# Kernel optimization log

Hardware: AMD Instinct MI355X
Metric: run time of the kernel (lower is better)

## Reference

```python
import jax, jax.numpy as jnp
import numpy as np

C = 128
K = 23
D = 3
ALPHA = 0.5
K_D = max(1, K // D)          # 7
S = 2 * D - 1                 # 5
C4 = C // 4 if C >= 4 else 1  # 32


def dwconv(x, w, pad, dil):
    # x: [B,C,H,W], w: [C,1,kh,kw] depthwise (groups=C)
    return jax.lax.conv_general_dilated(
        x, w, window_strides=(1, 1), padding=pad, rhs_dilation=dil,
        dimension_numbers=('NCHW', 'OIHW', 'NCHW'),
        feature_group_count=x.shape[1])


def setup_inputs() -> dict:
    key = jax.random.key(0)
    ks = jax.random.split(key, 10)
    sc = 0.1
    return {
        'x': jax.random.normal(ks[0], (4, C, 256, 256), jnp.float32),
        'h1_w': jax.random.normal(ks[1], (C, 1, 1, S), jnp.float32) * sc,
        'h2_w': jax.random.normal(ks[2], (C, 1, 1, K_D), jnp.float32) * sc,
        'v1_w': jax.random.normal(ks[3], (C, 1, S, 1), jnp.float32) * sc,
        'v2_w': jax.random.normal(ks[4], (C, 1, K_D, 1), jnp.float32) * sc,
        'g1_w': jax.random.normal(ks[5], (C4, 2 * C), jnp.float32) * sc,
        'g2_w': jax.random.normal(ks[6], (2, C4), jnp.float32) * sc,
        'g2_b': jnp.zeros((2,), jnp.float32),
        'fuse_w': jax.random.normal(ks[7], (C, C), jnp.float32) * sc,
        'fuse_b': jnp.zeros((C,), jnp.float32),
    }


def reference(x, h1_w, h2_w, v1_w, v2_w, g1_w, g2_w, g2_b, fuse_w, fuse_b):
    # directional depthwise large-kernel paths
    h = dwconv(x, h1_w, [(0, 0), (S // 2, S // 2)], (1, 1))
    h = dwconv(h, h2_w, [(0, 0), ((K_D - 1) * D // 2, (K_D - 1) * D // 2)], (1, D))
    v = dwconv(x, v1_w, [(S // 2, S // 2), (0, 0)], (1, 1))
    v = dwconv(v, v2_w, [((K_D - 1) * D // 2, (K_D - 1) * D // 2), (0, 0)], (D, 1))
    # gate: global avg pool over concat[h, v] -> 1x1 MLP -> softmax over 2 dirs
    pooled = jnp.concatenate([h.mean(axis=(2, 3)), v.mean(axis=(2, 3))], axis=1)  # [B, 2C]
    g = pooled @ g1_w.T
    g = g * jax.nn.sigmoid(g)  # SiLU
    w = jax.nn.softmax(g @ g2_w.T + g2_b, axis=1)  # [B, 2]
    wh = w[:, 0][:, None, None, None]
    wv = w[:, 1][:, None, None, None]
    attn = wh * h + wv * v
    # 1x1 fuse conv
    attn = jnp.einsum('bchw,oc->bohw', attn, fuse_w) + fuse_b[None, :, None, None]
    y = x * attn
    return x + ALPHA * (y - x)
```

## Files before the change

kernel.cpp:

```cpp
#include <hip/hip_runtime.h>
#include <hip/hip_bf16.h>

#define CCH 128
#define HGT 256
#define WID 256
#define HW  65536

typedef __attribute__((ext_vector_type(8))) short short8;
typedef __attribute__((ext_vector_type(4))) float floatx4;


__global__ __launch_bounds__(256) void prep_kernel(float* __restrict__ sums) {
  int t = threadIdx.x;
  for (int i = t; i < 1032; i += 256) sums[i] = 0.f;
}

__global__ __launch_bounds__(256) void convh_kernel(
    const float* __restrict__ x, const float* __restrict__ h1w,
    const float* __restrict__ h2w,
    __hip_bfloat16* __restrict__ hbuf, float* __restrict__ sum_h) {
  __shared__ float xr[16 * 260];
  __shared__ float tmp[16 * 276];
  __shared__ float red[4];
  int bid = blockIdx.x;
  int y0 = (bid & 15) * 16;
  int bc = bid >> 4;
  int c = bc & (CCH - 1);
  int t = threadIdx.x;
  int rowg = t >> 6;
  int c4 = (t & 63) * 4;

  if (t < 64) {
    int r = t >> 2, k = t & 3;
    int col = (k < 2) ? k : (256 + k);
    xr[r * 260 + col] = 0.f;
  }
  for (int i = t; i < 288; i += 256) {
    int r = i / 18, k = i - r * 18;
    int col = (k < 9) ? k : (256 + k);
    tmp[r * 276 + col] = 0.f;
  }

  const float* xg = x + (size_t)bc * HW + (size_t)y0 * WID;
#pragma unroll
  for (int k = 0; k < 4; ++k) {
    int r = 4 * k + rowg;
    float4 v = *(const float4*)(xg + (size_t)r * WID + c4);
    *(float2*)&xr[r * 260 + 2 + c4] = make_float2(v.x, v.y);
    *(float2*)&xr[r * 260 + 4 + c4] = make_float2(v.z, v.w);
  }
  float h1c[5], h2c[7];
#pragma unroll
  for (int i = 0; i < 5; ++i) h1c[i] = h1w[c * 5 + i];
#pragma unroll
  for (int j = 0; j < 7; ++j) h2c[j] = h2w[c * 7 + j];
  __syncthreads();

#pragma unroll
  for (int r = 0; r < 16; ++r) {
    float s1 = 0.f;
#pragma unroll
    for (int i = 0; i < 5; ++i) s1 = fmaf(xr[r * 260 + t + i], h1c[i], s1);
    tmp[r * 276 + 9 + t] = s1;
  }
  __syncthreads();

  __hip_bfloat16* hg = hbuf + (size_t)bc * HW + (size_t)y0 * WID + t;
  float acc = 0.f;
#pragma unroll
  for (int r = 0; r < 16; ++r) {
    float s = 0.f;
#pragma unroll
    for (int j = 0; j < 7; ++j) s = fmaf(tmp[r * 276 + t + 3 * j], h2c[j], s);
    hg[(size_t)r * WID] = __float2bfloat16(s);
    acc += s;
  }
#pragma unroll
  for (int off = 32; off > 0; off >>= 1) acc += __shfl_down(acc, off);
  if ((t & 63) == 0) red[t >> 6] = acc;
  __syncthreads();
  if (t == 0) atomicAdd(&sum_h[bc], red[0] + red[1] + red[2] + red[3]);
}

__global__ __launch_bounds__(256) void convv_kernel(
    const float* __restrict__ x, const float* __restrict__ v1w,
    const float* __restrict__ v2w,
    __hip_bfloat16* __restrict__ vbuf, float* __restrict__ sum_v) {
  int bid = blockIdx.x;
  int half = bid & 1;
  int bc = bid >> 1;
  int c = bc & (CCH - 1);
  int t = threadIdx.x;
  int y0 = half * 128;
  const float* xp = x + (size_t)bc * HW;
  float v1c[5], v2c[7];
#pragma unroll
  for (int i = 0; i < 5; ++i) v1c[i] = v1w[c * 5 + i];
#pragma unroll
  for (int j = 0; j < 7; ++j) v2c[j] = v2w[c * 7 + j];

  float xloc[23];
#pragma unroll
  for (int m = 0; m < 23; ++m) {
    int yy = y0 - 11 + m;
    xloc[m] = (yy >= 0 && yy < HGT) ? xp[(size_t)yy * WID + t] : 0.f;
  }
  float s1w[19];
#pragma unroll
  for (int m = 0; m < 19; ++m) {
    int q = y0 - 9 + m;
    float v = 0.f;
    if (q >= 0 && q < HGT) {
#pragma unroll
      for (int i = 0; i < 5; ++i) v = fmaf(xloc[m + i], v1c[i], v);
    }
    s1w[m] = v;
  }
  float xw[5];
#pragma unroll
  for (int i = 0; i < 5; ++i) {
    int yy = y0 + 8 + i;
    xw[i] = (yy >= 0 && yy < HGT) ? xp[(size_t)yy * WID + t] : 0.f;
  }

  __hip_bfloat16* vp = vbuf + (size_t)bc * HW;
  float acc = 0.f;
  for (int y = y0; y < y0 + 128; ++y) {
    float s = 0.f;
#pragma unroll
    for (int j = 0; j < 7; ++j) s = fmaf(s1w[3 * j], v2c[j], s);
    vp[(size_t)y * WID + t] = __float2bfloat16(s);
    acc += s;
#pragma unroll
    for (int m = 0; m < 18; ++m) s1w[m] = s1w[m + 1];
    int q = y + 10;
    float ns = 0.f;
    if (q < HGT) {
#pragma unroll
      for (int i = 0; i < 5; ++i) ns = fmaf(xw[i], v1c[i], ns);
    }
    s1w[18] = ns;
#pragma unroll
    for (int i = 0; i < 4; ++i) xw[i] = xw[i + 1];
    int yy = y + 13;
    xw[4] = (yy < HGT) ? xp[(size_t)yy * WID + t] : 0.f;
  }
  __shared__ float red[4];
#pragma unroll
  for (int off = 32; off > 0; off >>= 1) acc += __shfl_down(acc, off);
  if ((t & 63) == 0) red[t >> 6] = acc;
  __syncthreads();
  if (t == 0) atomicAdd(&sum_v[bc], red[0] + red[1] + red[2] + red[3]);
}

__global__ __launch_bounds__(128) void gate_kernel(
    const float* __restrict__ sum_h, const float* __restrict__ sum_v,
    const float* __restrict__ g1w, const float* __restrict__ g2w,
    const float* __restrict__ g2b, float* __restrict__ wgate) {
  int t = threadIdx.x;
  __shared__ float gs[4][32];
  int b = t >> 5, r = t & 31;
  {
    float acc = 0.f;
    const float inv = 1.f / 65536.f;
    for (int k = 0; k < 128; ++k)
      acc = fmaf(sum_h[b * 128 + k] * inv, g1w[r * 256 + k], acc);
    for (int k = 0; k < 128; ++k)
      acc = fmaf(sum_v[b * 128 + k] * inv, g1w[r * 256 + 128 + k], acc);
    float sig = 1.f / (1.f + expf(-acc));
    gs[b][r] = acc * sig;
  }
  __syncthreads();
  if (t < 4) {
    float t0 = g2b[0], t1 = g2b[1];
    for (int rr = 0; rr < 32; ++rr) {
      t0 = fmaf(gs[t][rr], g2w[rr], t0);
      t1 = fmaf(gs[t][rr], g2w[32 + rr], t1);
    }
    float mx = fmaxf(t0, t1);
    float e0 = expf(t0 - mx), e1 = expf(t1 - mx);
    float inv = 1.f / (e0 + e1);
    wgate[t * 2 + 0] = e0 * inv;
    wgate[t * 2 + 1] = e1 * inv;
  }
}

__device__ __forceinline__ float bf2f(unsigned short u) {
  return __uint_as_float(((unsigned)u) << 16);
}
__device__ __forceinline__ short f2bfs(float f) {
  return (short)__bfloat16_as_ushort(__float2bfloat16(f));
}

__global__ __launch_bounds__(256, 4) void fuse_kernel(
    const float* __restrict__ x, const __hip_bfloat16* __restrict__ hbuf,
    const __hip_bfloat16* __restrict__ vbuf, const float* __restrict__ fuse_w,
    const float* __restrict__ fuse_b, const float* __restrict__ wgate,
    float* __restrict__ out) {
  __shared__ unsigned short aT[128 * 128];
  int bid = blockIdx.x;
  int half = bid & 1;
  int y = (bid >> 1) & 255;
  int b = bid >> 9;
  int t = threadIdx.x;
  int w = t >> 6, lane = t & 63;
  int quad = lane >> 4, n16 = lane & 15;
  float wh = wgate[b * 2], wv = wgate[b * 2 + 1];

  short8 wf[2][4];
#pragma unroll
  for (int mi = 0; mi < 2; ++mi) {
    int o = (2 * w + mi) * 16 + n16;
#pragma unroll
    for (int kt = 0; kt < 4; ++kt) {
      const float* wp = fuse_w + o * 128 + kt * 32 + quad * 8;
      float4 f0 = *(const float4*)wp;
      float4 f1 = *(const float4*)(wp + 4);
      short8 s;
      s[0] = f2bfs(f0.x); s[1] = f2bfs(f0.y); s[2] = f2bfs(f0.z); s[3] = f2bfs(f0.w);
      s[4] = f2bfs(f1.x); s[5] = f2bfs(f1.y); s[6] = f2bfs(f1.z); s[7] = f2bfs(f1.w);
      wf[mi][kt] = s;
    }
  }

  size_t base = (size_t)(b * CCH) * HW + (size_t)y * WID + half * 128;
  const unsigned short* hb = (const unsigned short*)hbuf;
  const unsigned short* vb = (const unsigned short*)vbuf;
  int cth = t >> 4;
  int p0 = (t & 15) * 8;
  int swz = 8 * (t & 15);
#pragma unroll
  for (int cpass = 0; cpass < 8; ++cpass) {
    int c = cpass * 16 + cth;
    size_t gi = base + (size_t)c * HW + p0;
    ushort4 h0 = *(const ushort4*)(hb + gi);
    ushort4 h1 = *(const ushort4*)(hb + gi + 4);
    ushort4 v0 = *(const ushort4*)(vb + gi);
    ushort4 v1 = *(const ushort4*)(vb + gi + 4);
    int cpr = (c + swz) & 127;
    float a0 = fmaf(wh, bf2f(h0.x), wv * bf2f(v0.x));
    float a1 = fmaf(wh, bf2f(h0.y), wv * bf2f(v0.y));
    float a2 = fmaf(wh, bf2f(h0.z), wv * bf2f(v0.z));
    float a3 = fmaf(wh, bf2f(h0.w), wv * bf2f(v0.w));
    float a4 = fmaf(wh, bf2f(h1.x), wv * bf2f(v1.x));
    float a5 = fmaf(wh, bf2f(h1.y), wv * bf2f(v1.y));
    float a6 = fmaf(wh, bf2f(h1.z), wv * bf2f(v1.z));
    float a7 = fmaf(wh, bf2f(h1.w), wv * bf2f(v1.w));
    aT[(p0 + 0) * 128 + cpr] = (unsigned short)f2bfs(a0);
    aT[(p0 + 1) * 128 + cpr] = (unsigned short)f2bfs(a1);
    aT[(p0 + 2) * 128 + cpr] = (unsigned short)f2bfs(a2);
    aT[(p0 + 3) * 128 + cpr] = (unsigned short)f2bfs(a3);
    aT[(p0 + 4) * 128 + cpr] = (unsigned short)f2bfs(a4);
    aT[(p0 + 5) * 128 + cpr] = (unsigned short)f2bfs(a5);
    aT[(p0 + 6) * 128 + cpr] = (unsigned short)f2bfs(a6);
    aT[(p0 + 7) * 128 + cpr] = (unsigned short)f2bfs(a7);
  }
  __syncthreads();

  floatx4 acc[2][8];
#pragma unroll
  for (int mi = 0; mi < 2; ++mi)
#pragma unroll
    for (int nt = 0; nt < 8; ++nt) acc[mi][nt] = (floatx4)0.f;

#pragma unroll
  for (int kt = 0; kt < 4; ++kt) {
#pragma unroll
    for (int nt = 0; nt < 8; ++nt) {
      int p = nt * 16 + n16;
      int cpr = (kt * 32 + quad * 8 + 8 * ((p >> 3) & 15)) & 127;
      short8 bfr = *(const short8*)&aT[p * 128 + cpr];
      acc[0][nt] = __builtin_amdgcn_mfma_f32_16x16x32_bf16(wf[0][kt], bfr, acc[0][nt], 0, 0, 0);
      acc[1][nt] = __builtin_amdgcn_mfma_f32_16x16x32_bf16(wf[1][kt], bfr, acc[1][nt], 0, 0, 0);
    }
  }

#pragma unroll
  for (int mi = 0; mi < 2; ++mi) {
    int ob = (2 * w + mi) * 16 + quad * 4;
#pragma unroll
    for (int r = 0; r < 4; ++r) {
      int o = ob + r;
      float fb = fuse_b[o];
      size_t gb = base + (size_t)o * HW + n16;
#pragma unroll
      for (int nt = 0; nt < 8; ++nt) {
        size_t gi = gb + nt * 16;
        float attn = fb + acc[mi][nt][r];
        out[gi] = x[gi] * fmaf(0.5f, attn, 0.5f);
      }
    }
  }
}

extern "C" void kernel_launch(void* const* d_in, const int* in_sizes, int n_in,
                              void* d_out, int out_size, void* d_ws, size_t ws_size,
                              hipStream_t stream) {
  const float* x      = (const float*)d_in[0];
  const float* h1w    = (const float*)d_in[1];
  const float* h2w    = (const float*)d_in[2];
  const float* v1w    = (const float*)d_in[3];
  const float* v2w    = (const float*)d_in[4];
  const float* g1w    = (const float*)d_in[5];
  const float* g2w    = (const float*)d_in[6];
  const float* g2b    = (const float*)d_in[7];
  const float* fusew  = (const float*)d_in[8];
  const float* fuseb  = (const float*)d_in[9];
  float* out = (float*)d_out;

  float* sums  = (float*)d_ws;
  float* sum_h = sums;
  float* sum_v = sums + 512;
  float* wgate = sums + 1024;
  __hip_bfloat16* hbuf = (__hip_bfloat16*)((char*)d_ws + 32768);
  __hip_bfloat16* vbuf = hbuf + (size_t)4 * CCH * HW;

  prep_kernel<<<1, 256, 0, stream>>>(sums);
  convh_kernel<<<4 * CCH * 16, 256, 0, stream>>>(x, h1w, h2w, hbuf, sum_h);
  convv_kernel<<<4 * CCH * 2, 256, 0, stream>>>(x, v1w, v2w, vbuf, sum_v);
  gate_kernel<<<1, 128, 0, stream>>>(sum_h, sum_v, g1w, g2w, g2b, wgate);
  fuse_kernel<<<4 * HGT * 2, 256, 0, stream>>>(x, hbuf, vbuf, fusew, fuseb, wgate, out);
}
```

Measured before the change: 428.6 us.

## Merge horizontal and vertical conv kernels into one register-tiled launch and restructure fuse

The separate horizontal and vertical depthwise conv kernels are replaced by one kernel with 32768 blocks. Horizontal blocks keep an 8-pixel register window per thread instead of using shared memory, and vertical blocks handle 8-row strips instead of serially sweeping 128 rows, which exposes much more parallelism. The blocks are interleaved so both directions run at the same time, and the block-level shared reduction becomes one atomic per wave. The fuse kernel now loads with 16-byte vectors, uses a different LDS swizzle, and splits the MFMA epilogue into two halves with x prefetched into registers. The cost is more atomics and redundant halo loads per block.

Measured after the change: 476.3 us. +11.1%, slower.

```diff
diff --git a/kernel.cpp b/kernel.cpp
--- a/kernel.cpp
+++ b/kernel.cpp
@@ -10,147 +10,112 @@
 typedef __attribute__((ext_vector_type(4))) float floatx4;
 
 
+__device__ __forceinline__ float bf2f(unsigned short u) {
+  return __uint_as_float(((unsigned)u) << 16);
+}
+__device__ __forceinline__ short f2bfs(float f) {
+  return (short)__bfloat16_as_ushort(__float2bfloat16(f));
+}
+
 __global__ __launch_bounds__(256) void prep_kernel(float* __restrict__ sums) {
   int t = threadIdx.x;
   for (int i = t; i < 1032; i += 256) sums[i] = 0.f;
 }
 
-__global__ __launch_bounds__(256) void convh_kernel(
-    const float* __restrict__ x, const float* __restrict__ h1w,
-    const float* __restrict__ h2w,
-    __hip_bfloat16* __restrict__ hbuf, float* __restrict__ sum_h) {
-  __shared__ float xr[16 * 260];
-  __shared__ float tmp[16 * 276];
-  __shared__ float red[4];
-  int bid = blockIdx.x;
-  int y0 = (bid & 15) * 16;
-  int bc = bid >> 4;
-  int c = bc & (CCH - 1);
-  int t = threadIdx.x;
-  int rowg = t >> 6;
-  int c4 = (t & 63) * 4;
-
-  if (t < 64) {
-    int r = t >> 2, k = t & 3;
-    int col = (k < 2) ? k : (256 + k);
-    xr[r * 260 + col] = 0.f;
-  }
-  for (int i = t; i < 288; i += 256) {
-    int r = i / 18, k = i - r * 18;
-    int col = (k < 9) ? k : (256 + k);
-    tmp[r * 276 + col] = 0.f;
-  }
-
-  const float* xg = x + (size_t)bc * HW + (size_t)y0 * WID;
-#pragma unroll
-  for (int k = 0; k < 4; ++k) {
-    int r = 4 * k + rowg;
-    float4 v = *(const float4*)(xg + (size_t)r * WID + c4);
-    *(float2*)&xr[r * 260 + 2 + c4] = make_float2(v.x, v.y);
-    *(float2*)&xr[r * 260 + 4 + c4] = make_float2(v.z, v.w);
-  }
-  float h1c[5], h2c[7];
-#pragma unroll
-  for (int i = 0; i < 5; ++i) h1c[i] = h1w[c * 5 + i];
-#pragma unroll
-  for (int j = 0; j < 7; ++j) h2c[j] = h2w[c * 7 + j];
-  __syncthreads();
-
-#pragma unroll
-  for (int r = 0; r < 16; ++r) {
-    float s1 = 0.f;
-#pragma unroll
-    for (int i = 0; i < 5; ++i) s1 = fmaf(xr[r * 260 + t + i], h1c[i], s1);
-    tmp[r * 276 + 9 + t] = s1;
-  }
-  __syncthreads();
-
-  __hip_bfloat16* hg = hbuf + (size_t)bc * HW + (size_t)y0 * WID + t;
-  float acc = 0.f;
-#pragma unroll
-  for (int r = 0; r < 16; ++r) {
-    float s = 0.f;
-#pragma unroll
-    for (int j = 0; j < 7; ++j) s = fmaf(tmp[r * 276 + t + 3 * j], h2c[j], s);
-    hg[(size_t)r * WID] = __float2bfloat16(s);
-    acc += s;
+__global__ __launch_bounds__(256, 4) void conv_kernel(
+    const float* __restrict__ x,
+    const float* __restrict__ h1w, const float* __restrict__ h2w,
+    const float* __restrict__ v1w, const float* __restrict__ v2w,
+    __hip_bfloat16* __restrict__ hbuf, __hip_bfloat16* __restrict__ vbuf,
+    float* __restrict__ sum_h, float* __restrict__ sum_v) {
+  int d = blockIdx.x;
+  int l = (d & 7) * 4096 + (d >> 3);
+  int t = threadIdx.x;
+  float acc;
+  int bcg;
+  float* sums;
+  if (l < 16384) {
+    int bc = l >> 5;
+    int c = bc & (CCH - 1);
+    int row = (l & 31) * 8 + (t >> 5);
+    int p0 = (t & 31) * 8;
+    const float* xr = x + (size_t)bc * HW + (size_t)row * WID;
+    float w1[5], w2[7];
+#pragma unroll
+    for (int i = 0; i < 5; ++i) w1[i] = h1w[c * 5 + i];
+#pragma unroll
+    for (int j = 0; j < 7; ++j) w2[j] = h2w[c * 7 + j];
+    float xv[32];
+#pragma unroll
+    for (int k = 0; k < 8; ++k) {
+      int col = p0 - 12 + 4 * k;
+      float4 v = make_float4(0.f, 0.f, 0.f, 0.f);
+      if (col >= 0 && col < WID) v = *(const float4*)(xr + col);
+      xv[4 * k] = v.x; xv[4 * k + 1] = v.y; xv[4 * k + 2] = v.z; xv[4 * k + 3] = v.w;
+    }
+    float s1[26];
+#pragma unroll
+    for (int m = 0; m < 26; ++m) {
+      int q = p0 - 9 + m;
+      float s = 0.f;
+#pragma unroll
+      for (int i = 0; i < 5; ++i) s = fmaf(xv[m + 1 + i], w1[i], s);
+      s1[m] = ((unsigned)q < (unsigned)WID) ? s : 0.f;
+    }
+    short8 st;
+    acc = 0.f;
+#pragma unroll
+    for (int u = 0; u < 8; ++u) {
+      float s = 0.f;
+#pragma unroll
+      for (int j = 0; j < 7; ++j) s = fmaf(s1[u + 3 * j], w2[j], s);
+      st[u] = f2bfs(s);
+      acc += s;
+    }
+    *(short8*)((unsigned short*)hbuf + (size_t)bc * HW + (size_t)row * WID + p0) = st;
+    bcg = bc; sums = sum_h;
+  } else {
+    int lb = l - 16384;
+    int bc = lb >> 5;
+    int c = bc & (CCH - 1);
+    int y0 = (lb & 31) * 8;
+    int col = t;
+    const float* xc = x + (size_t)bc * HW + col;
+    float w1[5], w2[7];
+#pragma unroll
+    for (int i = 0; i < 5; ++i) w1[i] = v1w[c * 5 + i];
+#pragma unroll
+    for (int j = 0; j < 7; ++j) w2[j] = v2w[c * 7 + j];
+    float xv[30];
+#pragma unroll
+    for (int m = 0; m < 30; ++m) {
+      int yy = y0 - 11 + m;
+      xv[m] = ((unsigned)yy < (unsigned)HGT) ? xc[(size_t)yy * WID] : 0.f;
+    }
+    float s1[26];
+#pragma unroll
+    for (int m = 0; m < 26; ++m) {
+      int q = y0 - 9 + m;
+      float s = 0.f;
+#pragma unroll
+      for (int i = 0; i < 5; ++i) s = fmaf(xv[m + i], w1[i], s);
+      s1[m] = ((unsigned)q < (unsigned)HGT) ? s : 0.f;
+    }
+    unsigned short* vp = (unsigned short*)vbuf + (size_t)bc * HW + col;
+    acc = 0.f;
+#pragma unroll
+    for (int u = 0; u < 8; ++u) {
+      float s = 0.f;
+#pragma unroll
+      for (int j = 0; j < 7; ++j) s = fmaf(s1[u + 3 * j], w2[j], s);
+      vp[(size_t)(y0 + u) * WID] = (unsigned short)f2bfs(s);
+      acc += s;
+    }
+    bcg = bc; sums = sum_v;
   }
 #pragma unroll
   for (int off = 32; off > 0; off >>= 1) acc += __shfl_down(acc, off);
-  if ((t & 63) == 0) red[t >> 6] = acc;
-  __syncthreads();
-  if (t == 0) atomicAdd(&sum_h[bc], red[0] + red[1] + red[2] + red[3]);
-}
-
-__global__ __launch_bounds__(256) void convv_kernel(
-    const float* __restrict__ x, const float* __restrict__ v1w,
-    const float* __restrict__ v2w,
-    __hip_bfloat16* __restrict__ vbuf, float* __restrict__ sum_v) {
-  int bid = blockIdx.x;
-  int half = bid & 1;
-  int bc = bid >> 1;
-  int c = bc & (CCH - 1);
-  int t = threadIdx.x;
-  int y0 = half * 128;
-  const float* xp = x + (size_t)bc * HW;
-  float v1c[5], v2c[7];
-#pragma unroll
-  for (int i = 0; i < 5; ++i) v1c[i] = v1w[c * 5 + i];
-#pragma unroll
-  for (int j = 0; j < 7; ++j) v2c[j] = v2w[c * 7 + j];
-
-  float xloc[23];
-#pragma unroll
-  for (int m = 0; m < 23; ++m) {
-    int yy = y0 - 11 + m;
-    xloc[m] = (yy >= 0 && yy < HGT) ? xp[(size_t)yy * WID + t] : 0.f;
-  }
-  float s1w[19];
-#pragma unroll
-  for (int m = 0; m < 19; ++m) {
-    int q = y0 - 9 + m;
-    float v = 0.f;
-    if (q >= 0 && q < HGT) {
-#pragma unroll
-      for (int i = 0; i < 5; ++i) v = fmaf(xloc[m + i], v1c[i], v);
-    }
-    s1w[m] = v;
-  }
-  float xw[5];
-#pragma unroll
-  for (int i = 0; i < 5; ++i) {
-    int yy = y0 + 8 + i;
-    xw[i] = (yy >= 0 && yy < HGT) ? xp[(size_t)yy * WID + t] : 0.f;
-  }
-
-  __hip_bfloat16* vp = vbuf + (size_t)bc * HW;
-  float acc = 0.f;
-  for (int y = y0; y < y0 + 128; ++y) {
-    float s = 0.f;
-#pragma unroll
-    for (int j = 0; j < 7; ++j) s = fmaf(s1w[3 * j], v2c[j], s);
-    vp[(size_t)y * WID + t] = __float2bfloat16(s);
-    acc += s;
-#pragma unroll
-    for (int m = 0; m < 18; ++m) s1w[m] = s1w[m + 1];
-    int q = y + 10;
-    float ns = 0.f;
-    if (q < HGT) {
-#pragma unroll
-      for (int i = 0; i < 5; ++i) ns = fmaf(xw[i], v1c[i], ns);
-    }
-    s1w[18] = ns;
-#pragma unroll
-    for (int i = 0; i < 4; ++i) xw[i] = xw[i + 1];
-    int yy = y + 13;
-    xw[4] = (yy < HGT) ? xp[(size_t)yy * WID + t] : 0.f;
-  }
-  __shared__ float red[4];
-#pragma unroll
-  for (int off = 32; off > 0; off >>= 1) acc += __shfl_down(acc, off);
-  if ((t & 63) == 0) red[t >> 6] = acc;
-  __syncthreads();
-  if (t == 0) atomicAdd(&sum_v[bc], red[0] + red[1] + red[2] + red[3]);
+  if ((t & 63) == 0) atomicAdd(&sums[bcg], acc);
 }
 
 __global__ __launch_bounds__(128) void gate_kernel(
@@ -185,13 +150,6 @@
   }
 }
 
-__device__ __forceinline__ float bf2f(unsigned short u) {
-  return __uint_as_float(((unsigned)u) << 16);
-}
-__device__ __forceinline__ short f2bfs(float f) {
-  return (short)__bfloat16_as_ushort(__float2bfloat16(f));
-}
-
 __global__ __launch_bounds__(256, 4) void fuse_kernel(
     const float* __restrict__ x, const __hip_bfloat16* __restrict__ hbuf,
     const __hip_bfloat16* __restrict__ vbuf, const float* __restrict__ fuse_w,
@@ -228,68 +186,72 @@
   const unsigned short* vb = (const unsigned short*)vbuf;
   int cth = t >> 4;
   int p0 = (t & 15) * 8;
-  int swz = 8 * (t & 15);
-#pragma unroll
-  for (int cpass = 0; cpass < 8; ++cpass) {
-    int c = cpass * 16 + cth;
-    size_t gi = base + (size_t)c * HW + p0;
-    ushort4 h0 = *(const ushort4*)(hb + gi);
-    ushort4 h1 = *(const ushort4*)(hb + gi + 4);
-    ushort4 v0 = *(const ushort4*)(vb + gi);
-    ushort4 v1 = *(const ushort4*)(vb + gi + 4);
-    int cpr = (c + swz) & 127;
-    float a0 = fmaf(wh, bf2f(h0.x), wv * bf2f(v0.x));
-    float a1 = fmaf(wh, bf2f(h0.y), wv * bf2f(v0.y));
-    float a2 = fmaf(wh, bf2f(h0.z), wv * bf2f(v0.z));
-    float a3 = fmaf(wh, bf2f(h0.w), wv * bf2f(v0.w));
-    float a4 = fmaf(wh, bf2f(h1.x), wv * bf2f(v1.x));
-    float a5 = fmaf(wh, bf2f(h1.y), wv * bf2f(v1.y));
-    float a6 = fmaf(wh, bf2f(h1.z), wv * bf2f(v1.z));
-    float a7 = fmaf(wh, bf2f(h1.w), wv * bf2f(v1.w));
-    aT[(p0 + 0) * 128 + cpr] = (unsigned short)f2bfs(a0);
-    aT[(p0 + 1) * 128 + cpr] = (unsigned short)f2bfs(a1);
-    aT[(p0 + 2) * 128 + cpr] = (unsigned short)f2bfs(a2);
-    aT[(p0 + 3) * 128 + cpr] = (unsigned short)f2bfs(a3);
-    aT[(p0 + 4) * 128 + cpr] = (unsigned short)f2bfs(a4);
-    aT[(p0 + 5) * 128 + cpr] = (unsigned short)f2bfs(a5);
-    aT[(p0 + 6) * 128 + cpr] = (unsigned short)f2bfs(a6);
-    aT[(p0 + 7) * 128 + cpr] = (unsigned short)f2bfs(a7);
+#pragma unroll 1
+  for (int rnd = 0; rnd < 2; ++rnd) {
+    short8 hv[8];
+#pragma unroll
+    for (int cp = 0; cp < 4; ++cp) {
+      int c = (rnd * 4 + cp) * 16 + cth;
+      size_t gi = base + (size_t)c * HW + p0;
+      hv[2 * cp]     = *(const short8*)(hb + gi);
+      hv[2 * cp + 1] = *(const short8*)(vb + gi);
+    }
+#pragma unroll
+    for (int cp = 0; cp < 4; ++cp) {
+      int c = (rnd * 4 + cp) * 16 + cth;
+#pragma unroll
+      for (int e = 0; e < 8; ++e) {
+        float a = fmaf(wh, bf2f((unsigned short)hv[2 * cp][e]),
+                       wv * bf2f((unsigned short)hv[2 * cp + 1][e]));
+        int p = p0 + e;
+        int cpr = (c + 8 * ((p >> 2) & 15)) & 127;
+        aT[p * 128 + cpr] = (unsigned short)f2bfs(a);
+      }
+    }
   }
   __syncthreads();
 
-  floatx4 acc[2][8];
-#pragma unroll
-  for (int mi = 0; mi < 2; ++mi)
-#pragma unroll
-    for (int nt = 0; nt < 8; ++nt) acc[mi][nt] = (floatx4)0.f;
-
-#pragma unroll
-  for (int kt = 0; kt < 4; ++kt) {
-#pragma unroll
-    for (int nt = 0; nt < 8; ++nt) {
-      int p = nt * 16 + n16;
-      int cpr = (kt * 32 + quad * 8 + 8 * ((p >> 3) & 15)) & 127;
-      short8 bfr = *(const short8*)&aT[p * 128 + cpr];
-      acc[0][nt] = __builtin_amdgcn_mfma_f32_16x16x32_bf16(wf[0][kt], bfr, acc[0][nt], 0, 0, 0);
-      acc[1][nt] = __builtin_amdgcn_mfma_f32_16x16x32_bf16(wf[1][kt], bfr, acc[1][nt], 0, 0, 0);
-    }
-  }
-
-#pragma unroll
-  for (int mi = 0; mi < 2; ++mi) {
-    int ob = (2 * w + mi) * 16 + quad * 4;
-#pragma unroll
-    for (int r = 0; r < 4; ++r) {
-      int o = ob + r;
-      float fb = fuse_b[o];
-      size_t gb = base + (size_t)o * HW + n16;
-#pragma unroll
-      for (int nt = 0; nt < 8; ++nt) {
-        size_t gi = gb + nt * 16;
-        float attn = fb + acc[mi][nt][r];
-        out[gi] = x[gi] * fmaf(0.5f, attn, 0.5f);
-      }
-    }
+#pragma unroll 1
+  for (int hf = 0; hf < 2; ++hf) {
+    float xp[32];
+#pragma unroll
+    for (int mi = 0; mi < 2; ++mi)
+#pragma unroll
+      for (int r = 0; r < 4; ++r) {
+        int o = (2 * w + mi) * 16 + quad * 4 + r;
+        size_t gb = base + (size_t)o * HW + hf * 64 + n16;
+#pragma unroll
+        for (int ntl = 0; ntl < 4; ++ntl)
+          xp[(mi * 4 + r) * 4 + ntl] = x[gb + ntl * 16];
+      }
+    floatx4 acc[2][4];
+#pragma unroll
+    for (int mi = 0; mi < 2; ++mi)
+#pragma unroll
+      for (int ntl = 0; ntl < 4; ++ntl) acc[mi][ntl] = (floatx4)0.f;
+#pragma unroll
+    for (int kt = 0; kt < 4; ++kt)
+#pragma unroll
+      for (int ntl = 0; ntl < 4; ++ntl) {
+        int p = (hf * 4 + ntl) * 16 + n16;
+        int cpr = (kt * 32 + quad * 8 + 8 * ((p >> 2) & 15)) & 127;
+        short8 bfr = *(const short8*)&aT[p * 128 + cpr];
+        acc[0][ntl] = __builtin_amdgcn_mfma_f32_16x16x32_bf16(wf[0][kt], bfr, acc[0][ntl], 0, 0, 0);
+        acc[1][ntl] = __builtin_amdgcn_mfma_f32_16x16x32_bf16(wf[1][kt], bfr, acc[1][ntl], 0, 0, 0);
+      }
+#pragma unroll
+    for (int mi = 0; mi < 2; ++mi)
+#pragma unroll
+      for (int r = 0; r < 4; ++r) {
+        int o = (2 * w + mi) * 16 + quad * 4 + r;
+        float fb = fuse_b[o];
+        size_t gb = base + (size_t)o * HW + hf * 64 + n16;
+#pragma unroll
+        for (int ntl = 0; ntl < 4; ++ntl) {
+          float attn = fb + acc[mi][ntl][r];
+          out[gb + ntl * 16] = xp[(mi * 4 + r) * 4 + ntl] * fmaf(0.5f, attn, 0.5f);
+        }
+      }
   }
 }
 
@@ -316,8 +278,7 @@
   __hip_bfloat16* vbuf = hbuf + (size_t)4 * CCH * HW;
 
   prep_kernel<<<1, 256, 0, stream>>>(sums);
-  convh_kernel<<<4 * CCH * 16, 256, 0, stream>>>(x, h1w, h2w, hbuf, sum_h);
-  convv_kernel<<<4 * CCH * 2, 256, 0, stream>>>(x, v1w, v2w, vbuf, sum_v);
+  conv_kernel<<<32768, 256, 0, stream>>>(x, h1w, h2w, v1w, v2w, hbuf, vbuf, sum_h, sum_v);
   gate_kernel<<<1, 128, 0, stream>>>(sum_h, sum_v, g1w, g2w, g2b, wgate);
   fuse_kernel<<<4 * HGT * 2, 256, 0, stream>>>(x, hbuf, vbuf, fusew, fuseb, wgate, out);
 }
```
